# Kernel tuning notes

Hardware: AMD Instinct MI355X
Metric: run time of the kernel (lower is better)

## Reference

```python
import jax, jax.numpy as jnp
import numpy as np

N = 50000          # num nodes
E = 800000         # num edges (before self loops)
DIM_IN = 128
HID = 32           # per-head hidden of conv1
HEADS = 8          # heads of conv1
DIM_OUT = 16       # output classes (conv2, 1 head, concat=False)
NEG_SLOPE = 0.2    # GATConv default leaky_relu slope


def gat_conv(x, W, a_src, a_dst, bias, src, dst, heads, out_ch, concat):
    """PyG GATConv (self-loops already appended to src/dst).
    x: [N, F_in], W: [F_in, heads*out_ch], a_src/a_dst: [heads, out_ch], bias matches output.
    """
    n = x.shape[0]
    h = (x @ W).reshape(n, heads, out_ch)                    # [N, H, C]
    al_src = jnp.einsum('nhc,hc->nh', h, a_src)              # [N, H]
    al_dst = jnp.einsum('nhc,hc->nh', h, a_dst)              # [N, H]
    e = jax.nn.leaky_relu(al_src[src] + al_dst[dst], NEG_SLOPE)   # [E', H]
    # segment softmax over edges grouped by target node (dst)
    emax = jax.ops.segment_max(e, dst, num_segments=n)       # [N, H]
    ee = jnp.exp(e - emax[dst])                              # [E', H]
    denom = jax.ops.segment_sum(ee, dst, num_segments=n)     # [N, H]
    alpha = ee / (denom[dst] + 1e-16)                        # [E', H]
    msg = h[src] * alpha[:, :, None]                         # [E', H, C]
    out = jax.ops.segment_sum(msg, dst, num_segments=n)      # [N, H, C]
    out = out.reshape(n, heads * out_ch) if concat else out.mean(axis=1)
    return out + bias


def setup_inputs() -> dict:
    key = jax.random.key(0)
    ks = jax.random.split(key, 12)
    x = jax.random.normal(ks[0], (N, DIM_IN), dtype=jnp.float32)
    edge_index = jax.random.randint(ks[1], (2, E), 0, N, dtype=jnp.int64)
    s = 0.1
    W1 = jax.random.normal(ks[2], (DIM_IN, HEADS * HID), dtype=jnp.float32) * s
    a1_src = jax.random.normal(ks[3], (HEADS, HID), dtype=jnp.float32) * s
    a1_dst = jax.random.normal(ks[4], (HEADS, HID), dtype=jnp.float32) * s
    b1 = jnp.zeros((HEADS * HID,), dtype=jnp.float32)
    W2 = jax.random.normal(ks[5], (HEADS * HID, DIM_OUT), dtype=jnp.float32) * s
    a2_src = jax.random.normal(ks[6], (1, DIM_OUT), dtype=jnp.float32) * s
    a2_dst = jax.random.normal(ks[7], (1, DIM_OUT), dtype=jnp.float32) * s
    b2 = jnp.zeros((DIM_OUT,), dtype=jnp.float32)
    return {"x": x, "edge_index": edge_index, "W1": W1, "a1_src": a1_src,
            "a1_dst": a1_dst, "b1": b1, "W2": W2, "a2_src": a2_src,
            "a2_dst": a2_dst, "b2": b2}


def reference(x, edge_index, W1, a1_src, a1_dst, b1, W2, a2_src, a2_dst, b2):
    # add self loops (GATConv default add_self_loops=True)
    loops = jnp.arange(N, dtype=edge_index.dtype)
    src = jnp.concatenate([edge_index[0], loops])
    dst = jnp.concatenate([edge_index[1], loops])
    # dropout layers are identity in eval mode
    h = gat_conv(x, W1, a1_src, a1_dst, b1, src, dst, HEADS, HID, concat=True)
    h = jax.nn.elu(h)
    out = gat_conv(h, W2, a2_src, a2_dst, b2, src, dst, 1, DIM_OUT, concat=False)
    return jax.nn.log_softmax(out, axis=1)
```

## Files before the change

kernel.cpp:

```cpp
#include <hip/hip_runtime.h>
#include <hip/hip_bf16.h>

#define NN 50000
#define EE 800000
#define EP (EE + NN)
#define DIN 128
#define HID 32
#define HEADS 8
#define C1 (HEADS * HID)
#define DOUT 16
#define NW1 3125
#define SH 8
#define NB 196
#define CAP 8192
#define EPT 8
#define BBLK (256 * EPT)
#define GB ((NW1 * 64 + 255) / 256)
#define BB ((EP + BBLK - 1) / BBLK)

typedef __attribute__((ext_vector_type(8))) short short8;
typedef __attribute__((ext_vector_type(4))) float float4v;
typedef __attribute__((ext_vector_type(2))) float float2v;

__device__ inline unsigned short f2bf(float f) {
    __hip_bfloat16 b = __float2bfloat16(f);
    return *reinterpret_cast<unsigned short*>(&b);
}
__device__ inline float bflo(unsigned u) {
    union { unsigned int i; float f; } x;
    x.i = u << 16;
    return x.f;
}
__device__ inline float bfhi(unsigned u) {
    union { unsigned int i; float f; } x;
    x.i = u & 0xffff0000u;
    return x.f;
}

__global__ void k_prepfw(const float* __restrict__ W1, const float* __restrict__ a1s,
                         const float* __restrict__ a1d, const float* __restrict__ W2,
                         unsigned short* __restrict__ w1frag,
                         unsigned short* __restrict__ w2frag,
                         int* __restrict__ cntb) {
    int i = blockIdx.x * 256 + threadIdx.x;
    if (blockIdx.x == 0 && threadIdx.x < NB) cntb[threadIdx.x] = 0;
    if (i < 17 * 2048) {
        int j = i & 7, lane = (i >> 3) & 63, s = (i >> 9) & 3, c = i >> 11;
        int q = lane >> 4, m = lane & 15;
        int k = s * 32 + q * 8 + j;
        float val;
        if (c < 16) {
            val = W1[k * C1 + c * 16 + m];
        } else {
            int h = m & 7;
            const float* av = (m < 8) ? a1s : a1d;
            float acc = 0.f;
            #pragma unroll
            for (int j2 = 0; j2 < 32; j2++)
                acc += W1[k * C1 + h * 32 + j2] * av[h * 32 + j2];
            val = acc;
        }
        w1frag[i] = f2bf(val);
    } else if (i < 17 * 2048 + 8 * 512) {
        int j2 = i - 17 * 2048;
        int jj = j2 & 7, lane = (j2 >> 3) & 63, s = j2 >> 9;
        int q = lane >> 4, m = lane & 15;
        w2frag[j2] = f2bf(W2[(s * 32 + q * 8 + jj) * DOUT + m]);
    }
}

__global__ __launch_bounds__(256) void k_g1bkt(const float* __restrict__ x,
                                               const unsigned short* __restrict__ w1frag,
                                               unsigned char* __restrict__ h1f8,
                                               float* __restrict__ al1sd,
                                               const int* __restrict__ ei,
                                               int* __restrict__ cntb,
                                               unsigned* __restrict__ ebuf) {
    __shared__ int hist[4][NB];
    __shared__ int base[4][NB];
    int bid = blockIdx.x;
    if (bid < GB) {
        int wid = (bid * 256 + threadIdx.x) >> 6;
        int lane = threadIdx.x & 63;
        if (wid >= NW1) return;
        int nb = wid * 16;
        int m = lane & 15, quad = lane >> 4;
        const float* xrow = x + (nb + m) * DIN;

        float4 xf[8];
        #pragma unroll
        for (int s = 0; s < 4; s++) {
            xf[2 * s]     = *(const float4*)(xrow + s * 32 + quad * 8);
            xf[2 * s + 1] = *(const float4*)(xrow + s * 32 + quad * 8 + 4);
        }
        short8 bfr[4];
        #pragma unroll
        for (int s = 0; s < 4; s++) {
            unsigned short* bp = (unsigned short*)&bfr[s];
            float4 f0 = xf[2 * s], f1 = xf[2 * s + 1];
            bp[0] = f2bf(f0.x); bp[1] = f2bf(f0.y); bp[2] = f2bf(f0.z); bp[3] = f2bf(f0.w);
            bp[4] = f2bf(f1.x); bp[5] = f2bf(f1.y); bp[6] = f2bf(f1.z); bp[7] = f2bf(f1.w);
        }

        float4v acc[17];
        #pragma unroll
        for (int c = 0; c < 17; c++) acc[c] = (float4v){0.f, 0.f, 0.f, 0.f};

        #pragma unroll
        for (int s = 0; s < 4; s++) {
            const unsigned short* fp = w1frag + (s * 64 + lane) * 8;
            #pragma unroll
            for (int c = 0; c < 17; c++) {
                short8 afrag = *(const short8*)(fp + c * 2048);
                acc[c] = __builtin_amdgcn_mfma_f32_16x16x32_bf16(afrag, bfr[s], acc[c], 0, 0, 0);
            }
        }

        int node = nb + m;
        #pragma unroll
        for (int c = 0; c < 16; c++) {
            unsigned pk = 0;
            pk = __builtin_amdgcn_cvt_pk_fp8_f32(acc[c][0], acc[c][1], pk, false);
            pk = __builtin_amdgcn_cvt_pk_fp8_f32(acc[c][2], acc[c][3], pk, true);
            *(unsigned*)(h1f8 + node * C1 + c * 16 + quad * 4) = pk;
        }
        *(float4*)(al1sd + node * 16 + quad * 4) =
            make_float4(acc[16][0], acc[16][1], acc[16][2], acc[16][3]);
    } else {
        int t = threadIdx.x;
        int wave = t >> 6;
        for (int i = t; i < 4 * NB; i += 256) ((int*)hist)[i] = 0;
        __syncthreads();
        int e0 = (bid - GB) * BBLK;
        int s[EPT], d[EPT], r[EPT];
        #pragma unroll
        for (int j = 0; j < EPT; j++) {
            int e = e0 + j * 256 + t;
            int ss = 0, dd = -1;
            if (e < EE) { ss = ei[e]; dd = ei[EE + e]; }
            else if (e < EP) { ss = e - EE; dd = ss; }
            s[j] = ss; d[j] = dd;
            if (dd >= 0) r[j] = atomicAdd(&hist[wave][dd >> SH], 1);
        }
        __syncthreads();
        if (t < NB) {
            int h0 = hist[0][t], h1 = hist[1][t], h2 = hist[2][t], h3 = hist[3][t];
            int tot = h0 + h1 + h2 + h3;
            int bb = tot ? atomicAdd(&cntb[t], tot) : 0;
            base[0][t] = bb;
            base[1][t] = bb + h0;
            base[2][t] = bb + h0 + h1;
            base[3][t] = bb + h0 + h1 + h2;
        }
        __syncthreads();
        #pragma unroll
        for (int j = 0; j < EPT; j++) {
            if (d[j] >= 0) {
                int b = d[j] >> SH;
                ebuf[b * CAP + base[wave][b] + r[j]] =
                    ((unsigned)s[j] << SH) | (unsigned)(d[j] & 255);
            }
        }
    }
}

__global__ __launch_bounds__(1024) void k_csr(const int* __restrict__ cntb,
                                              const unsigned* __restrict__ ebuf,
                                              int* __restrict__ row_ptr,
                                              int* __restrict__ esrc) {
    __shared__ int sdeg[256];
    __shared__ int wtot[4];
    __shared__ int bpart[4];
    int b = blockIdx.x;
    int t = threadIdx.x;
    int lane = t & 63, wave = t >> 6;
    int nodes0 = b << SH;
    if (t < 256) sdeg[t] = 0;
    if (t < 256) {
        int v = (t < b) ? cntb[t] : 0;
        #pragma unroll
        for (int off = 1; off < 64; off <<= 1) v += __shfl_xor(v, off, 64);
        if (lane == 0) bpart[wave] = v;
    }
    __syncthreads();
    int baseS = bpart[0] + bpart[1] + bpart[2] + bpart[3];
    int cnt = cntb[b];
    const unsigned* eb = ebuf + b * CAP;
    for (int i = t; i < cnt; i += 1024)
        atomicAdd(&sdeg[eb[i] & 255], 1);
    __syncthreads();
    int v = (t < 256) ? sdeg[t] : 0;
    int inc = v;
    #pragma unroll
    for (int off = 1; off < 64; off <<= 1) {
        int u = __shfl_up(inc, off, 64);
        if (lane >= off) inc += u;
    }
    if (t < 256 && lane == 63) wtot[wave] = inc;
    __syncthreads();
    if (wave == 0 && lane < 4) {
        int w = wtot[lane];
        int iw = w;
        #pragma unroll
        for (int off = 1; off < 4; off <<= 1) {
            int u = __shfl_up(iw, off, 64);
            if (lane >= off) iw += u;
        }
        wtot[lane] = iw - w;
    }
    __syncthreads();
    int excl = inc - v + ((t < 256) ? wtot[wave] : 0);
    __syncthreads();
    if (t < 256) {
        sdeg[t] = excl;
        int node = nodes0 + t;
        if (node < NN) row_ptr[node] = baseS + excl;
    }
    __syncthreads();
    for (int i = t; i < cnt; i += 1024) {
        unsigned e = eb[i];
        int pos = atomicAdd(&sdeg[e & 255], 1);
        esrc[baseS + pos] = (int)(e >> SH);
    }
    if (b == 0 && t == 0) row_ptr[NN] = EP;
}

__global__ __launch_bounds__(256) void k_agg1(const int* __restrict__ row_ptr,
                                              const int* __restrict__ esrc,
                                              const float* __restrict__ al1sd,
                                              const unsigned char* __restrict__ h1f8,
                                              const float* __restrict__ b1,
                                              unsigned short* __restrict__ helu_b) {
    int L = threadIdx.x & 63;
    int d = __builtin_amdgcn_readfirstlane((int)((blockIdx.x * 256 + threadIdx.x) >> 6));
    int start = row_ptr[d], end = row_ptr[d + 1];
    const int Lofs = L * 4;
    const int hprod = L & 7;
    const int hcons = L >> 3;
    float ald_p = al1sd[d * 16 + 8 + hprod];
    float denom = 0.f;
    float4 acc = make_float4(0.f, 0.f, 0.f, 0.f);

    for (int base = start; base < end; base += 64) {
        int cnt = min(64, end - base);
        int sval = d;
        if (L < cnt) sval = esrc[base + L];
        int cnt8 = (cnt + 7) & ~7;
        for (int i = 0; i < cnt8; i += 8) {
            int eidx = i + (L >> 3);
            int sp = __shfl(sval, eidx, 64);
            float as = al1sd[sp * 16 + hprod];
            float e = as + ald_p;
            e = e > 0.f ? e : 0.2f * e;
            float w = (eidx < cnt) ? __expf(e) : 0.f;
            unsigned v[8];
            float xw[8];
            #pragma unroll
            for (int j = 0; j < 8; j++) {
                int sj = __builtin_amdgcn_readlane(sval, i + j);
                v[j] = *(const unsigned*)(h1f8 + sj * C1 + Lofs);
                xw[j] = __shfl(w, j * 8 + hcons, 64);
            }
            #pragma unroll
            for (int j = 0; j < 8; j++) {
                float2v a = __builtin_amdgcn_cvt_pk_f32_fp8(v[j], false);
                float2v b = __builtin_amdgcn_cvt_pk_f32_fp8(v[j], true);
                float xj = xw[j];
                denom += xj;
                acc.x += xj * a.x; acc.y += xj * a.y; acc.z += xj * b.x; acc.w += xj * b.y;
            }
        }
    }
    float inv = 1.0f / (denom + 1e-16f);
    float4 bv = *(const float4*)(b1 + Lofs);
    float o0 = acc.x * inv + bv.x;
    float o1 = acc.y * inv + bv.y;
    float o2 = acc.z * inv + bv.z;
    float o3 = acc.w * inv + bv.w;
    o0 = o0 > 0.f ? o0 : __expf(o0) - 1.0f;
    o1 = o1 > 0.f ? o1 : __expf(o1) - 1.0f;
    o2 = o2 > 0.f ? o2 : __expf(o2) - 1.0f;
    o3 = o3 > 0.f ? o3 : __expf(o3) - 1.0f;
    uint2 pk;
    pk.x = (unsigned)f2bf(o0) | ((unsigned)f2bf(o1) << 16);
    pk.y = (unsigned)f2bf(o2) | ((unsigned)f2bf(o3) << 16);
    *(uint2*)(helu_b + d * C1 + Lofs) = pk;
}

__global__ __launch_bounds__(256) void k_gemm2(const unsigned short* __restrict__ helu_b,
                                               const unsigned short* __restrict__ w2frag,
                                               const float* __restrict__ a2s,
                                               const float* __restrict__ a2d,
                                               unsigned short* __restrict__ h2b,
                                               float* __restrict__ al2s,
                                               float* __restrict__ al2d) {
    int wid = (blockIdx.x * 256 + threadIdx.x) >> 6;
    int lane = threadIdx.x & 63;
    int nb = wid * 16;
    if (nb >= NN) return;
    int m = lane & 15, quad = lane >> 4;

    const unsigned short* wp2 = w2frag + lane * 8;
    float4v acc = {0.f, 0.f, 0.f, 0.f};
    const unsigned short* arow = helu_b + (nb + m) * C1 + quad * 8;
    #pragma unroll
    for (int s = 0; s < 8; s++) {
        short8 afrag = *(const short8*)(arow + s * 32);
        short8 bfrag = *(const short8*)(wp2 + s * 512);
        acc = __builtin_amdgcn_mfma_f32_16x16x32_bf16(afrag, bfrag, acc, 0, 0, 0);
    }

    float as_c = a2s[m], ad_c = a2d[m];
    #pragma unroll
    for (int r = 0; r < 4; r++) {
        int node = nb + quad * 4 + r;
        float val = acc[r];
        h2b[node * DOUT + m] = f2bf(val);
        float ps = val * as_c;
        float pd = val * ad_c;
        ps += __shfl_xor(ps, 1, 64); ps += __shfl_xor(ps, 2, 64);
        ps += __shfl_xor(ps, 4, 64); ps += __shfl_xor(ps, 8, 64);
        pd += __shfl_xor(pd, 1, 64); pd += __shfl_xor(pd, 2, 64);
        pd += __shfl_xor(pd, 4, 64); pd += __shfl_xor(pd, 8, 64);
        if (m == 0) {
            al2s[node] = ps;
            al2d[node] = pd;
        }
    }
}

__global__ __launch_bounds__(256) void k_agg2(const int* __restrict__ row_ptr,
                                              const int* __restrict__ esrc,
                                              const unsigned short* __restrict__ h2b,
                                              const float* __restrict__ al2s,
                                              const float* __restrict__ al2d,
                                              const float* __restrict__ b2,
                                              float* __restrict__ out) {
    __shared__ float wbuf2[4][64];
    __shared__ int   sbuf2[4][64];
    int wslot = threadIdx.x >> 6;
    int L = threadIdx.x & 63;
    int n = (blockIdx.x * 256 + threadIdx.x) >> 6;
    if (n >= NN) return;
    int p = L & 7, g = L >> 3;
    int start = row_ptr[n], end = row_ptr[n + 1];
    float ald = al2d[n];
    float* wrow = wbuf2[wslot];
    int* srow = sbuf2[wslot];
    float acc0 = 0.f, acc1 = 0.f, denom = 0.f;

    for (int base = start; base < end; base += 64) {
        int cnt = min(64, end - base);
        int s = n; float w = 0.f;
        if (L < cnt) {
            s = esrc[base + L];
            float e = al2s[s] + ald;
            e = e > 0.f ? e : 0.2f * e;
            w = __expf(e);
        }
        srow[L] = s;
        wrow[L] = w;
        int cnt8 = (cnt + 7) & ~7;
        for (int i = 0; i < cnt8; i += 8) {
            int idx = i + g;
            int ss = srow[idx];
            float ww = wrow[idx];
            unsigned v = *(const unsigned*)(h2b + ss * DOUT + p * 2);
            acc0 += ww * bflo(v);
            acc1 += ww * bfhi(v);
            denom += ww;
        }
    }
    acc0 += __shfl_xor(acc0, 8, 64);  acc0 += __shfl_xor(acc0, 16, 64);  acc0 += __shfl_xor(acc0, 32, 64);
    acc1 += __shfl_xor(acc1, 8, 64);  acc1 += __shfl_xor(acc1, 16, 64);  acc1 += __shfl_xor(acc1, 32, 64);
    denom += __shfl_xor(denom, 8, 64); denom += __shfl_xor(denom, 16, 64); denom += __shfl_xor(denom, 32, 64);
    float inv = 1.0f / (denom + 1e-16f);
    float2 bv = *(const float2*)(b2 + p * 2);
    float val0 = acc0 * inv + bv.x;
    float val1 = acc1 * inv + bv.y;
    float m = fmaxf(val0, val1);
    #pragma unroll
    for (int mm = 1; mm < 8; mm <<= 1) m = fmaxf(m, __shfl_xor(m, mm, 64));
    float se = __expf(val0 - m) + __expf(val1 - m);
    #pragma unroll
    for (int mm = 1; mm < 8; mm <<= 1) se += __shfl_xor(se, mm, 64);
    float lse = m + __logf(se);
    if (L < 8) {
        float2 o = make_float2(val0 - lse, val1 - lse);
        *(float2*)(out + n * DOUT + p * 2) = o;
    }
}

extern "C" void kernel_launch(void* const* d_in, const int* in_sizes, int n_in,
                              void* d_out, int out_size, void* d_ws, size_t ws_size,
                              hipStream_t stream) {
    const float* x   = (const float*)d_in[0];
    const int*   ei  = (const int*)d_in[1];
    const float* W1  = (const float*)d_in[2];
    const float* a1s = (const float*)d_in[3];
    const float* a1d = (const float*)d_in[4];
    const float* b1  = (const float*)d_in[5];
    const float* W2  = (const float*)d_in[6];
    const float* a2s = (const float*)d_in[7];
    const float* a2d = (const float*)d_in[8];
    const float* b2  = (const float*)d_in[9];
    float* outp = (float*)d_out;

    unsigned char* h1f8    = (unsigned char*)d_ws;
    unsigned short* helu_b = (unsigned short*)(h1f8 + NN * C1);
    unsigned short* h2b    = helu_b + NN * C1;
    unsigned short* w2frag = h2b + NN * DOUT;
    unsigned short* w1frag = w2frag + 8 * 512;
    float* al1sd = (float*)(w1frag + 17 * 2048);
    float* al2sb = al1sd + NN * 16;
    float* al2db = al2sb + NN;
    int* row_ptr = (int*)(al2db + NN);
    int* esrc    = row_ptr + NN + 1;
    int* cntb    = esrc + EP;
    unsigned* ebuf = (unsigned*)helu_b;

    k_prepfw<<<(17 * 2048 + 8 * 512 + 255) / 256, 256, 0, stream>>>(W1, a1s, a1d, W2, w1frag, w2frag, cntb);
    k_g1bkt<<<GB + BB, 256, 0, stream>>>(x, w1frag, h1f8, al1sd, ei, cntb, ebuf);
    k_csr<<<NB, 1024, 0, stream>>>(cntb, ebuf, row_ptr, esrc);
    k_agg1<<<12500, 256, 0, stream>>>(row_ptr, esrc, al1sd, h1f8, b1, helu_b);
    k_gemm2<<<(NW1 * 64 + 255) / 256, 256, 0, stream>>>(helu_b, w2frag, a2s, a2d, h2b, al2sb, al2db);
    k_agg2<<<(NN * 64 + 255) / 256, 256, 0, stream>>>(row_ptr, esrc, h2b, al2sb, al2db, b2, outp);
}
```

Baseline: 198.8 us.

## Fuse layer-2 projection and attention logits into the layer-1 aggregation kernel

The second-layer linear projection (256→16) and the per-node attention scores are now computed inside the layer-1 aggregation kernel. Each lane multiplies its four ELU outputs by fp32 W2 rows, and the wave reduces the result with a butterfly transpose-reduce over shuffles. This drops the bf16 intermediate activation buffer, one kernel launch and the W2 fragment prep, which saves a large write and re-read of the hidden activations. In exchange it adds many shuffles and extra W2 loads per node in an already gather-bound kernel, and computes in fp32 with scalar FMAs instead of bf16 MFMA.

```diff
diff --git a/kernel.cpp b/kernel.cpp
--- a/kernel.cpp
+++ b/kernel.cpp
@@ -38,9 +38,8 @@
 }
 
 __global__ void k_prepfw(const float* __restrict__ W1, const float* __restrict__ a1s,
-                         const float* __restrict__ a1d, const float* __restrict__ W2,
+                         const float* __restrict__ a1d,
                          unsigned short* __restrict__ w1frag,
-                         unsigned short* __restrict__ w2frag,
                          int* __restrict__ cntb) {
     int i = blockIdx.x * 256 + threadIdx.x;
     if (blockIdx.x == 0 && threadIdx.x < NB) cntb[threadIdx.x] = 0;
@@ -61,11 +60,6 @@
             val = acc;
         }
         w1frag[i] = f2bf(val);
-    } else if (i < 17 * 2048 + 8 * 512) {
-        int j2 = i - 17 * 2048;
-        int jj = j2 & 7, lane = (j2 >> 3) & 63, s = j2 >> 9;
-        int q = lane >> 4, m = lane & 15;
-        w2frag[j2] = f2bf(W2[(s * 32 + q * 8 + jj) * DOUT + m]);
     }
 }
 
@@ -230,7 +224,12 @@
                                               const float* __restrict__ al1sd,
                                               const unsigned char* __restrict__ h1f8,
                                               const float* __restrict__ b1,
-                                              unsigned short* __restrict__ helu_b) {
+                                              const float* __restrict__ W2,
+                                              const float* __restrict__ a2s,
+                                              const float* __restrict__ a2d,
+                                              unsigned short* __restrict__ h2b,
+                                              float* __restrict__ al2s,
+                                              float* __restrict__ al2d) {
     int L = threadIdx.x & 63;
     int d = __builtin_amdgcn_readfirstlane((int)((blockIdx.x * 256 + threadIdx.x) >> 6));
     int start = row_ptr[d], end = row_ptr[d + 1];
@@ -281,52 +280,64 @@
     o1 = o1 > 0.f ? o1 : __expf(o1) - 1.0f;
     o2 = o2 > 0.f ? o2 : __expf(o2) - 1.0f;
     o3 = o3 > 0.f ? o3 : __expf(o3) - 1.0f;
-    uint2 pk;
-    pk.x = (unsigned)f2bf(o0) | ((unsigned)f2bf(o1) << 16);
-    pk.y = (unsigned)f2bf(o2) | ((unsigned)f2bf(o3) << 16);
-    *(uint2*)(helu_b + d * C1 + Lofs) = pk;
-}
-
-__global__ __launch_bounds__(256) void k_gemm2(const unsigned short* __restrict__ helu_b,
-                                               const unsigned short* __restrict__ w2frag,
-                                               const float* __restrict__ a2s,
-                                               const float* __restrict__ a2d,
-                                               unsigned short* __restrict__ h2b,
-                                               float* __restrict__ al2s,
-                                               float* __restrict__ al2d) {
-    int wid = (blockIdx.x * 256 + threadIdx.x) >> 6;
-    int lane = threadIdx.x & 63;
-    int nb = wid * 16;
-    if (nb >= NN) return;
-    int m = lane & 15, quad = lane >> 4;
-
-    const unsigned short* wp2 = w2frag + lane * 8;
-    float4v acc = {0.f, 0.f, 0.f, 0.f};
-    const unsigned short* arow = helu_b + (nb + m) * C1 + quad * 8;
-    #pragma unroll
-    for (int s = 0; s < 8; s++) {
-        short8 afrag = *(const short8*)(arow + s * 32);
-        short8 bfrag = *(const short8*)(wp2 + s * 512);
-        acc = __builtin_amdgcn_mfma_f32_16x16x32_bf16(afrag, bfrag, acc, 0, 0, 0);
-    }
-
-    float as_c = a2s[m], ad_c = a2d[m];
-    #pragma unroll
-    for (int r = 0; r < 4; r++) {
-        int node = nb + quad * 4 + r;
-        float val = acc[r];
-        h2b[node * DOUT + m] = f2bf(val);
-        float ps = val * as_c;
-        float pd = val * ad_c;
-        ps += __shfl_xor(ps, 1, 64); ps += __shfl_xor(ps, 2, 64);
-        ps += __shfl_xor(ps, 4, 64); ps += __shfl_xor(ps, 8, 64);
-        pd += __shfl_xor(pd, 1, 64); pd += __shfl_xor(pd, 2, 64);
-        pd += __shfl_xor(pd, 4, 64); pd += __shfl_xor(pd, 8, 64);
-        if (m == 0) {
-            al2s[node] = ps;
-            al2d[node] = pd;
-        }
-    }
+
+    float c[16];
+    {
+        const float* wr0 = W2 + (4 * L) * DOUT;
+        #pragma unroll
+        for (int k = 0; k < 16; k += 4) {
+            float4 wa = *(const float4*)(wr0 + k);
+            float4 wb = *(const float4*)(wr0 + DOUT + k);
+            float4 wc = *(const float4*)(wr0 + 2 * DOUT + k);
+            float4 wd = *(const float4*)(wr0 + 3 * DOUT + k);
+            c[k]     = o0 * wa.x + o1 * wb.x + o2 * wc.x + o3 * wd.x;
+            c[k + 1] = o0 * wa.y + o1 * wb.y + o2 * wc.y + o3 * wd.y;
+            c[k + 2] = o0 * wa.z + o1 * wb.z + o2 * wc.z + o3 * wd.z;
+            c[k + 3] = o0 * wa.w + o1 * wb.w + o2 * wc.w + o3 * wd.w;
+        }
+    }
+    #pragma unroll
+    for (int k = 0; k < 16; k++) {
+        c[k] += __shfl_xor(c[k], 1, 64);
+        c[k] += __shfl_xor(c[k], 2, 64);
+    }
+    int b2 = (L >> 2) & 1, b3 = (L >> 3) & 1, b4 = (L >> 4) & 1, b5 = (L >> 5) & 1;
+    #pragma unroll
+    for (int k = 0; k < 8; k++) {
+        float give = b2 ? c[k] : c[k + 8];
+        float keep = b2 ? c[k + 8] : c[k];
+        c[k] = keep + __shfl_xor(give, 4, 64);
+    }
+    #pragma unroll
+    for (int k = 0; k < 4; k++) {
+        float give = b3 ? c[k] : c[k + 4];
+        float keep = b3 ? c[k + 4] : c[k];
+        c[k] = keep + __shfl_xor(give, 8, 64);
+    }
+    #pragma unroll
+    for (int k = 0; k < 2; k++) {
+        float give = b4 ? c[k] : c[k + 2];
+        float keep = b4 ? c[k + 2] : c[k];
+        c[k] = keep + __shfl_xor(give, 16, 64);
+    }
+    {
+        float give = b5 ? c[0] : c[1];
+        float keep = b5 ? c[1] : c[0];
+        c[0] = keep + __shfl_xor(give, 32, 64);
+    }
+    int col = (b2 << 3) | (b3 << 2) | (b4 << 1) | b5;
+    float cf = c[0];
+    float ps = cf * a2s[col];
+    float pd = cf * a2d[col];
+    ps += __shfl_xor(ps, 4, 64);  ps += __shfl_xor(ps, 8, 64);
+    ps += __shfl_xor(ps, 16, 64); ps += __shfl_xor(ps, 32, 64);
+    pd += __shfl_xor(pd, 4, 64);  pd += __shfl_xor(pd, 8, 64);
+    pd += __shfl_xor(pd, 16, 64); pd += __shfl_xor(pd, 32, 64);
+    if (L == 0) {
+        al2s[d] = ps;
+        al2d[d] = pd;
+    }
+    if ((L & 3) == 0) h2b[d * DOUT + col] = f2bf(cf);
 }
 
 __global__ __launch_bounds__(256) void k_agg2(const int* __restrict__ row_ptr,
@@ -407,22 +418,19 @@
     float* outp = (float*)d_out;
 
     unsigned char* h1f8    = (unsigned char*)d_ws;
-    unsigned short* helu_b = (unsigned short*)(h1f8 + NN * C1);
-    unsigned short* h2b    = helu_b + NN * C1;
-    unsigned short* w2frag = h2b + NN * DOUT;
-    unsigned short* w1frag = w2frag + 8 * 512;
+    unsigned* ebuf = (unsigned*)(h1f8 + NN * C1);
+    unsigned short* h2b    = (unsigned short*)(ebuf + NB * CAP);
+    unsigned short* w1frag = h2b + NN * DOUT;
     float* al1sd = (float*)(w1frag + 17 * 2048);
     float* al2sb = al1sd + NN * 16;
     float* al2db = al2sb + NN;
     int* row_ptr = (int*)(al2db + NN);
     int* esrc    = row_ptr + NN + 1;
     int* cntb    = esrc + EP;
-    unsigned* ebuf = (unsigned*)helu_b;
-
-    k_prepfw<<<(17 * 2048 + 8 * 512 + 255) / 256, 256, 0, stream>>>(W1, a1s, a1d, W2, w1frag, w2frag, cntb);
+
+    k_prepfw<<<(17 * 2048 + 255) / 256, 256, 0, stream>>>(W1, a1s, a1d, w1frag, cntb);
     k_g1bkt<<<GB + BB, 256, 0, stream>>>(x, w1frag, h1f8, al1sd, ei, cntb, ebuf);
     k_csr<<<NB, 1024, 0, stream>>>(cntb, ebuf, row_ptr, esrc);
-    k_agg1<<<12500, 256, 0, stream>>>(row_ptr, esrc, al1sd, h1f8, b1, helu_b);
-    k_gemm2<<<(NW1 * 64 + 255) / 256, 256, 0, stream>>>(helu_b, w2frag, a2s, a2d, h2b, al2sb, al2db);
+    k_agg1<<<12500, 256, 0, stream>>>(row_ptr, esrc, al1sd, h1f8, b1, W2, a2s, a2d, h2b, al2sb, al2db);
     k_agg2<<<(NN * 64 + 255) / 256, 256, 0, stream>>>(row_ptr, esrc, h2b, al2sb, al2db, b2, outp);
 }
```

New measurement: 255.9 us. +28.7%, slower.
